# Performance work log

Hardware: AMD Instinct MI355X
Metric: run time of the kernel (lower is better)

Reference implementation:

```python
import jax, jax.numpy as jnp
import numpy as np

B, N, MAX_DEG = 256, 512, 6
F_IN, H = 62, 128  # layers = [62, 128, 128]
NUM_DEG = MAX_DEG + 1  # degree buckets 0..6


def gather_neighbors(atoms, edges, maskvalue):
    # atoms [B,N,F], edges [B,N,D] with -1 padding -> [B,N,D,F]
    idx = jnp.maximum(edges, 0)
    neigh = jax.vmap(lambda a, e: a[e])(atoms, idx)
    return jnp.where(edges[..., None] < 0, jnp.asarray(maskvalue, atoms.dtype), neigh)


def nfp_conv(atoms, edges, W, b):
    # W [NUM_DEG, F_in, F_out], b [NUM_DEG, F_out]
    deg = jnp.sum(edges >= 0, axis=-1)  # [B,N]
    neigh = gather_neighbors(atoms, edges, 0.0)
    summed = neigh.sum(axis=2) + atoms  # include self, [B,N,F_in]
    out = jnp.zeros(summed.shape[:2] + (W.shape[-1],), summed.dtype)
    for d in range(NUM_DEG):  # small fixed set of degree buckets
        h = jax.nn.sigmoid(summed @ W[d] + b[d])
        out = out + h * (deg == d)[..., None].astype(h.dtype)
    return out


def graph_pool(atoms, edges):
    # max over self + neighbors
    neigh = gather_neighbors(atoms, edges, -jnp.inf)
    allf = jnp.concatenate([atoms[:, :, None, :], neigh], axis=2)  # [B,N,D+1,F]
    return allf.max(axis=2)


def setup_inputs() -> dict:
    key = jax.random.key(0)
    ka, ke, km, k0, k1, k2, k3 = jax.random.split(key, 7)
    a = jax.random.normal(ka, (B, N, F_IN), dtype=jnp.float32)
    e = jax.random.randint(ke, (B, N, MAX_DEG), 0, N, dtype=jnp.int32)
    # introduce -1 padding so atoms have varied degrees 0..6
    u = jax.random.uniform(km, (B, N, MAX_DEG))
    e = jnp.where(u < 0.6, e, -1).astype(jnp.int32)
    W0 = jax.random.normal(k0, (NUM_DEG, F_IN, H), dtype=jnp.float32) * 0.1
    b0 = jax.random.normal(k1, (NUM_DEG, H), dtype=jnp.float32) * 0.1
    W1 = jax.random.normal(k2, (NUM_DEG, H, H), dtype=jnp.float32) * 0.1
    b1 = jax.random.normal(k3, (NUM_DEG, H), dtype=jnp.float32) * 0.1
    return {"a": a, "e": e, "W0": W0, "b0": b0, "W1": W1, "b1": b1}


def reference(a, e, W0, b0, W1, b1):
    x = nfp_conv(a, e, W0, b0)
    x = graph_pool(x, e)
    x = nfp_conv(x, e, W1, b1)
    x = graph_pool(x, e)
    return x.sum(axis=1)  # SubgraphSum: [B, H]
```

## Files before the change

### kernel.cpp

```cpp
#include <hip/hip_runtime.h>
#include <math.h>

#define BB 256
#define NN 512
#define DD 6
#define F_IN 62
#define HH 128
#define ND 7
#define TOTAL (BB*NN)

typedef __bf16 bf16x8 __attribute__((ext_vector_type(8)));
typedef float f32x4 __attribute__((ext_vector_type(4)));

__device__ __forceinline__ unsigned short f2bf(float f) {
    unsigned u = __builtin_bit_cast(unsigned, f);
    u = (u + 0x7FFFu + ((u >> 16) & 1u)) >> 16;
    return (unsigned short)u;
}
__device__ __forceinline__ float lo2f(unsigned x) { return __builtin_bit_cast(float, x << 16); }
__device__ __forceinline__ float hi2f(unsigned x) { return __builtin_bit_cast(float, x & 0xFFFF0000u); }


__global__ void k_zero(unsigned int* ghist) {
    if (threadIdx.x < ND) ghist[threadIdx.x] = 0u;
}

__global__ __launch_bounds__(256) void k_hist(const int* __restrict__ e,
                                              int* __restrict__ deg,
                                              unsigned int* __restrict__ ghist) {
    __shared__ unsigned int lh[ND];
    int t = threadIdx.x;
    if (t < ND) lh[t] = 0u;
    __syncthreads();
    int u = blockIdx.x * 256 + t;
    int d = 0;
#pragma unroll
    for (int j = 0; j < DD; ++j) d += (e[u * DD + j] >= 0) ? 1 : 0;
    deg[u] = d;
    atomicAdd(&lh[d], 1u);
    __syncthreads();
    if (t < ND) atomicAdd(&ghist[t], lh[t]);
}

__global__ void k_scan(const unsigned int* __restrict__ ghist,
                       unsigned int* __restrict__ cursors) {
    unsigned int acc = 0;
    for (int d = 0; d < ND; ++d) { cursors[d] = acc; acc += ghist[d]; }
}

__global__ __launch_bounds__(256) void k_scatter(const int* __restrict__ deg,
                                                 int* __restrict__ order,
                                                 unsigned int* __restrict__ cursors) {
    __shared__ unsigned int lcnt[ND];
    __shared__ unsigned int lbase[ND];
    int t = threadIdx.x;
    if (t < ND) lcnt[t] = 0u;
    __syncthreads();
    int u = blockIdx.x * 256 + t;
    int d = deg[u];
    unsigned int r = atomicAdd(&lcnt[d], 1u);
    __syncthreads();
    if (t < ND) lbase[t] = atomicAdd(&cursors[t], lcnt[t]);
    __syncthreads();
    order[lbase[d] + r] = u;
}


__global__ __launch_bounds__(256) void k_prep_a(const float* __restrict__ a,
                                                unsigned short* __restrict__ Ap) {
    int u = blockIdx.x * 256 + threadIdx.x;
    int r = u >> 3;
    int c0 = (u & 7) * 8;
    unsigned short h[8];
#pragma unroll
    for (int i = 0; i < 8; ++i) {
        int c = c0 + i;
        h[i] = (c < F_IN) ? f2bf(a[(size_t)r * F_IN + c]) : (unsigned short)0;
    }
    uint4 p;
    p.x = (unsigned)h[0] | ((unsigned)h[1] << 16);
    p.y = (unsigned)h[2] | ((unsigned)h[3] << 16);
    p.z = (unsigned)h[4] | ((unsigned)h[5] << 16);
    p.w = (unsigned)h[6] | ((unsigned)h[7] << 16);
    *(uint4*)&Ap[(size_t)r * 64 + c0] = p;
}


__global__ void k_prep_wt(const float* __restrict__ W, unsigned short* __restrict__ WT,
                          int F, int K) {
    int n = blockIdx.x;
    int d = blockIdx.y;
    for (int k = threadIdx.x; k < K; k += 64) {
        float v = (k < F) ? W[((size_t)d * F + k) * HH + n] : 0.f;
        WT[((size_t)d * HH + n) * K + k] = f2bf(v);
    }
}


template<int KB>
__global__ __launch_bounds__(256, 3)
void k_conv_mfma(const unsigned short* __restrict__ Xp,
                 const int* __restrict__ e,
                 const unsigned short* __restrict__ WT,
                 const float* __restrict__ bias,
                 const int* __restrict__ order,
                 const int* __restrict__ deg,
                 unsigned short* __restrict__ Y) {
    constexpr int K = KB * 8;
    constexpr int LOGKB = (KB == 16) ? 4 : 3;
    __shared__ unsigned short sP[64 * 128];
    __shared__ int vT[64];
    __shared__ int degT[64];
    __shared__ int eT[64 * DD];

    const int t = threadIdx.x;
    const int l = t & 63;
    const int w = t >> 6;

    if (t < 64) {
        int v = order[blockIdx.x * 64 + t];
        vT[t] = v;
        degT[t] = deg[v];
    }
    __syncthreads();
    for (int i = t; i < 64 * DD; i += 256) eT[i] = e[vT[i / DD] * DD + (i % DD)];
    __syncthreads();

    for (int u = t; u < 64 * KB; u += 256) {
        const int kb = u & (KB - 1);
        const int n = u >> LOGKB;
        const int v = vT[n];
        const int nbase = v & ~(NN - 1);
        float s[8];
        {
            uint4 p = *(const uint4*)(Xp + (size_t)v * K + kb * 8);
            s[0] = lo2f(p.x); s[1] = hi2f(p.x); s[2] = lo2f(p.y); s[3] = hi2f(p.y);
            s[4] = lo2f(p.z); s[5] = hi2f(p.z); s[6] = lo2f(p.w); s[7] = hi2f(p.w);
        }
#pragma unroll
        for (int j = 0; j < DD; ++j) {
            int idx = eT[n * DD + j];
            if (idx >= 0) {
                uint4 p = *(const uint4*)(Xp + (size_t)(nbase + idx) * K + kb * 8);
                s[0] += lo2f(p.x); s[1] += hi2f(p.x); s[2] += lo2f(p.y); s[3] += hi2f(p.y);
                s[4] += lo2f(p.z); s[5] += hi2f(p.z); s[6] += lo2f(p.w); s[7] += hi2f(p.w);
            }
        }
        uint4 r;
        r.x = (unsigned)f2bf(s[0]) | ((unsigned)f2bf(s[1]) << 16);
        r.y = (unsigned)f2bf(s[2]) | ((unsigned)f2bf(s[3]) << 16);
        r.z = (unsigned)f2bf(s[4]) | ((unsigned)f2bf(s[5]) << 16);
        r.w = (unsigned)f2bf(s[6]) | ((unsigned)f2bf(s[7]) << 16);
        const int kbs = kb ^ (n & 7);
        *(uint4*)&sP[(n * KB + kbs) * 8] = r;
    }
    __syncthreads();

    const int dlo = degT[0];
    const int dhi = degT[63];
    const int lr = l & 15;
    const int lq = l >> 4;

    for (int d = dlo; d <= dhi; ++d) {
        bf16x8 bf[K / 32][2];
#pragma unroll
        for (int kk = 0; kk < K / 32; ++kk)
#pragma unroll
            for (int nb = 0; nb < 2; ++nb) {
                int ncol = w * 32 + nb * 16 + lr;
                int krow = kk * 32 + lq * 8;
                bf[kk][nb] = *(const bf16x8*)(WT + ((size_t)d * HH + ncol) * K + krow);
            }

        f32x4 acc[4][2];
#pragma unroll
        for (int mb = 0; mb < 4; ++mb)
#pragma unroll
            for (int nb = 0; nb < 2; ++nb) {
                f32x4 z = {0.f, 0.f, 0.f, 0.f};
                acc[mb][nb] = z;
            }

#pragma unroll
        for (int kk = 0; kk < K / 32; ++kk) {
#pragma unroll
            for (int mb = 0; mb < 4; ++mb) {
                int nrow = mb * 16 + lr;
                int kbp = kk * 4 + lq;
                int kbs = kbp ^ (nrow & 7);
                bf16x8 af = *(const bf16x8*)&sP[(nrow * KB + kbs) * 8];
                acc[mb][0] = __builtin_amdgcn_mfma_f32_16x16x32_bf16(af, bf[kk][0], acc[mb][0], 0, 0, 0);
                acc[mb][1] = __builtin_amdgcn_mfma_f32_16x16x32_bf16(af, bf[kk][1], acc[mb][1], 0, 0, 0);
            }
        }

        if (dlo == dhi) {
            __syncthreads();
#pragma unroll
            for (int mb = 0; mb < 4; ++mb)
#pragma unroll
                for (int nb = 0; nb < 2; ++nb) {
                    int col = w * 32 + nb * 16 + lr;
                    float bv = bias[d * HH + col];
#pragma unroll
                    for (int r = 0; r < 4; ++r) {
                        int n = mb * 16 + lq * 4 + r;
                        float z = 1.f / (1.f + __expf(-(acc[mb][nb][r] + bv)));
                        sP[n * HH + col] = f2bf(z);
                    }
                }
            __syncthreads();
            for (int u = t; u < 64 * HH / 8; u += 256) {
                int n = u >> 4;
                int c8 = (u & 15) * 8;
                uint4 p = *(const uint4*)&sP[n * HH + c8];
                *(uint4*)&Y[(size_t)vT[n] * HH + c8] = p;
            }
        } else {
#pragma unroll
            for (int mb = 0; mb < 4; ++mb)
#pragma unroll
                for (int nb = 0; nb < 2; ++nb) {
                    int col = w * 32 + nb * 16 + lr;
                    float bv = bias[d * HH + col];
#pragma unroll
                    for (int r = 0; r < 4; ++r) {
                        int n = mb * 16 + lq * 4 + r;
                        if (degT[n] == d) {
                            float z = 1.f / (1.f + __expf(-(acc[mb][nb][r] + bv)));
                            Y[(size_t)vT[n] * HH + col] = f2bf(z);
                        }
                    }
                }
        }
    }
}


__global__ __launch_bounds__(256) void k_pool_bf(const unsigned short* __restrict__ X,
                                                 const int* __restrict__ e,
                                                 unsigned short* __restrict__ P) {
    const int t = threadIdx.x;
    const int u = blockIdx.x * 16 + (t >> 4);
    const int c8 = (t & 15) * 8;
    const int nbase = u & ~(NN - 1);
    float m[8];
    {
        uint4 p = *(const uint4*)(X + (size_t)u * HH + c8);
        m[0] = lo2f(p.x); m[1] = hi2f(p.x); m[2] = lo2f(p.y); m[3] = hi2f(p.y);
        m[4] = lo2f(p.z); m[5] = hi2f(p.z); m[6] = lo2f(p.w); m[7] = hi2f(p.w);
    }
#pragma unroll
    for (int j = 0; j < DD; ++j) {
        int idx = e[u * DD + j];
        if (idx >= 0) {
            uint4 p = *(const uint4*)(X + (size_t)(nbase + idx) * HH + c8);
            m[0] = fmaxf(m[0], lo2f(p.x)); m[1] = fmaxf(m[1], hi2f(p.x));
            m[2] = fmaxf(m[2], lo2f(p.y)); m[3] = fmaxf(m[3], hi2f(p.y));
            m[4] = fmaxf(m[4], lo2f(p.z)); m[5] = fmaxf(m[5], hi2f(p.z));
            m[6] = fmaxf(m[6], lo2f(p.w)); m[7] = fmaxf(m[7], hi2f(p.w));
        }
    }
    uint4 r;
    r.x = (unsigned)f2bf(m[0]) | ((unsigned)f2bf(m[1]) << 16);
    r.y = (unsigned)f2bf(m[2]) | ((unsigned)f2bf(m[3]) << 16);
    r.z = (unsigned)f2bf(m[4]) | ((unsigned)f2bf(m[5]) << 16);
    r.w = (unsigned)f2bf(m[6]) | ((unsigned)f2bf(m[7]) << 16);
    *(uint4*)&P[(size_t)u * HH + c8] = r;
}


__global__ __launch_bounds__(256) void k_pool_sum_part(const unsigned short* __restrict__ X,
                                                       const int* __restrict__ e,
                                                       float* __restrict__ partial) {
    __shared__ float red[16][HH + 4];
    const int t = threadIdx.x;
    const int b = blockIdx.x >> 3;
    const int chunk = blockIdx.x & 7;
    const int slot = t >> 4;
    const int c8 = (t & 15) * 8;
    float acc[8];
#pragma unroll
    for (int i = 0; i < 8; ++i) acc[i] = 0.f;

    for (int n = chunk * 64 + slot; n < chunk * 64 + 64; n += 16) {
        int u = b * NN + n;
        float m[8];
        uint4 p = *(const uint4*)(X + (size_t)u * HH + c8);
        m[0] = lo2f(p.x); m[1] = hi2f(p.x); m[2] = lo2f(p.y); m[3] = hi2f(p.y);
        m[4] = lo2f(p.z); m[5] = hi2f(p.z); m[6] = lo2f(p.w); m[7] = hi2f(p.w);
#pragma unroll
        for (int j = 0; j < DD; ++j) {
            int idx = e[u * DD + j];
            if (idx >= 0) {
                uint4 q = *(const uint4*)(X + (size_t)(b * NN + idx) * HH + c8);
                m[0] = fmaxf(m[0], lo2f(q.x)); m[1] = fmaxf(m[1], hi2f(q.x));
                m[2] = fmaxf(m[2], lo2f(q.y)); m[3] = fmaxf(m[3], hi2f(q.y));
                m[4] = fmaxf(m[4], lo2f(q.z)); m[5] = fmaxf(m[5], hi2f(q.z));
                m[6] = fmaxf(m[6], lo2f(q.w)); m[7] = fmaxf(m[7], hi2f(q.w));
            }
        }
#pragma unroll
        for (int i = 0; i < 8; ++i) acc[i] += m[i];
    }
#pragma unroll
    for (int i = 0; i < 8; ++i) red[slot][c8 + i] = acc[i];
    __syncthreads();
    if (t < HH) {
        float s = 0.f;
#pragma unroll
        for (int k = 0; k < 16; ++k) s += red[k][t];
        partial[(size_t)blockIdx.x * HH + t] = s;
    }
}


__global__ __launch_bounds__(256) void k_sum_final(const float* __restrict__ partial,
                                                   float* __restrict__ out) {
    int g = blockIdx.x * 256 + threadIdx.x;
    int b = g >> 7;
    int c = g & 127;
    float s = 0.f;
#pragma unroll
    for (int k = 0; k < 8; ++k) s += partial[(size_t)(b * 8 + k) * HH + c];
    out[g] = s;
}


extern "C" void kernel_launch(void* const* d_in, const int* in_sizes, int n_in,
                              void* d_out, int out_size, void* d_ws, size_t ws_size,
                              hipStream_t stream) {
    const float* a  = (const float*)d_in[0];
    const int*   e  = (const int*)d_in[1];
    const float* W0 = (const float*)d_in[2];
    const float* b0 = (const float*)d_in[3];
    const float* W1 = (const float*)d_in[4];
    const float* b1 = (const float*)d_in[5];
    float* out = (float*)d_out;

    char* ws = (char*)d_ws;
    const size_t XB = (size_t)TOTAL * HH * 2;
    unsigned short* xbuf = (unsigned short*)ws;
    unsigned short* pbuf = (unsigned short*)(ws + XB);
    unsigned short* Ap   = (unsigned short*)(ws + 2 * XB);
    float* partial = (float*)Ap;
    unsigned short* WT0  = (unsigned short*)(ws + 2 * XB + (size_t)TOTAL * 64 * 2);
    unsigned short* WT1  = WT0 + (size_t)ND * HH * 64;
    char* ip = (char*)(WT1 + (size_t)ND * HH * 128);
    int* deg   = (int*)ip;
    int* order = (int*)(ip + (size_t)TOTAL * 4);
    unsigned int* ghist   = (unsigned int*)(ip + (size_t)TOTAL * 8);
    unsigned int* cursors = ghist + 8;

    hipLaunchKernelGGL(k_zero, dim3(1), dim3(64), 0, stream, ghist);
    hipLaunchKernelGGL(k_hist, dim3(TOTAL / 256), dim3(256), 0, stream, e, deg, ghist);
    hipLaunchKernelGGL(k_scan, dim3(1), dim3(1), 0, stream, ghist, cursors);
    hipLaunchKernelGGL(k_scatter, dim3(TOTAL / 256), dim3(256), 0, stream, deg, order, cursors);

    hipLaunchKernelGGL(k_prep_a, dim3(TOTAL * 8 / 256), dim3(256), 0, stream, a, Ap);
    hipLaunchKernelGGL(k_prep_wt, dim3(HH, ND), dim3(64), 0, stream, W0, WT0, F_IN, 64);
    hipLaunchKernelGGL(k_prep_wt, dim3(HH, ND), dim3(64), 0, stream, W1, WT1, HH, 128);

    hipLaunchKernelGGL((k_conv_mfma<8>),  dim3(TOTAL / 64), dim3(256), 0, stream,
                       Ap, e, WT0, b0, order, deg, xbuf);
    hipLaunchKernelGGL(k_pool_bf, dim3(TOTAL / 16), dim3(256), 0, stream, xbuf, e, pbuf);
    hipLaunchKernelGGL((k_conv_mfma<16>), dim3(TOTAL / 64), dim3(256), 0, stream,
                       pbuf, e, WT1, b1, order, deg, xbuf);
    hipLaunchKernelGGL(k_pool_sum_part, dim3(BB * 8), dim3(256), 0, stream, xbuf, e, partial);
    hipLaunchKernelGGL(k_sum_final, dim3(BB * HH / 256), dim3(256), 0, stream, partial, out);
}
```

Baseline: 170.5 us.

## Sort atoms by degree per batch and remap block IDs for XCD-local gathers

```diff
diff --git a/kernel.cpp b/kernel.cpp
--- a/kernel.cpp
+++ b/kernel.cpp
@@ -21,48 +21,28 @@
 __device__ __forceinline__ float hi2f(unsigned x) { return __builtin_bit_cast(float, x & 0xFFFF0000u); }
 
 
-__global__ void k_zero(unsigned int* ghist) {
-    if (threadIdx.x < ND) ghist[threadIdx.x] = 0u;
-}
-
-__global__ __launch_bounds__(256) void k_hist(const int* __restrict__ e,
-                                              int* __restrict__ deg,
-                                              unsigned int* __restrict__ ghist) {
+__global__ __launch_bounds__(512) void k_sort_batch(const int* __restrict__ e,
+                                                    int* __restrict__ deg,
+                                                    int* __restrict__ order) {
     __shared__ unsigned int lh[ND];
-    int t = threadIdx.x;
+    __shared__ unsigned int base[ND];
+    const int b = blockIdx.x;
+    const int t = threadIdx.x;
     if (t < ND) lh[t] = 0u;
     __syncthreads();
-    int u = blockIdx.x * 256 + t;
+    const int u = b * NN + t;
     int d = 0;
 #pragma unroll
     for (int j = 0; j < DD; ++j) d += (e[u * DD + j] >= 0) ? 1 : 0;
     deg[u] = d;
-    atomicAdd(&lh[d], 1u);
-    __syncthreads();
-    if (t < ND) atomicAdd(&ghist[t], lh[t]);
-}
-
-__global__ void k_scan(const unsigned int* __restrict__ ghist,
-                       unsigned int* __restrict__ cursors) {
-    unsigned int acc = 0;
-    for (int d = 0; d < ND; ++d) { cursors[d] = acc; acc += ghist[d]; }
-}
-
-__global__ __launch_bounds__(256) void k_scatter(const int* __restrict__ deg,
-                                                 int* __restrict__ order,
-                                                 unsigned int* __restrict__ cursors) {
-    __shared__ unsigned int lcnt[ND];
-    __shared__ unsigned int lbase[ND];
-    int t = threadIdx.x;
-    if (t < ND) lcnt[t] = 0u;
-    __syncthreads();
-    int u = blockIdx.x * 256 + t;
-    int d = deg[u];
-    unsigned int r = atomicAdd(&lcnt[d], 1u);
-    __syncthreads();
-    if (t < ND) lbase[t] = atomicAdd(&cursors[t], lcnt[t]);
-    __syncthreads();
-    order[lbase[d] + r] = u;
+    unsigned int r = atomicAdd(&lh[d], 1u);
+    __syncthreads();
+    if (t == 0) {
+        unsigned int acc = 0;
+        for (int k = 0; k < ND; ++k) { base[k] = acc; acc += lh[k]; }
+    }
+    __syncthreads();
+    order[b * NN + base[d] + r] = u;
 }
 
 
@@ -117,8 +97,15 @@
     const int l = t & 63;
     const int w = t >> 6;
 
+    const int bi = blockIdx.x;
+    const int x8 = bi & 7;
+    const int j = bi >> 3;
+    const int batch = x8 + 8 * (j >> 3);
+    const int tile = j & 7;
+    const int g0 = batch * NN + tile * 64;
+
     if (t < 64) {
-        int v = order[blockIdx.x * 64 + t];
+        int v = order[g0 + t];
         vT[t] = v;
         degT[t] = deg[v];
     }
@@ -138,8 +125,8 @@
             s[4] = lo2f(p.z); s[5] = hi2f(p.z); s[6] = lo2f(p.w); s[7] = hi2f(p.w);
         }
 #pragma unroll
-        for (int j = 0; j < DD; ++j) {
-            int idx = eT[n * DD + j];
+        for (int jj = 0; jj < DD; ++jj) {
+            int idx = eT[n * DD + jj];
             if (idx >= 0) {
                 uint4 p = *(const uint4*)(Xp + (size_t)(nbase + idx) * K + kb * 8);
                 s[0] += lo2f(p.x); s[1] += hi2f(p.x); s[2] += lo2f(p.y); s[3] += hi2f(p.y);
@@ -241,7 +228,12 @@
                                                  const int* __restrict__ e,
                                                  unsigned short* __restrict__ P) {
     const int t = threadIdx.x;
-    const int u = blockIdx.x * 16 + (t >> 4);
+    const int bi = blockIdx.x;
+    const int x8 = bi & 7;
+    const int j = bi >> 3;
+    const int batch = x8 + 8 * (j >> 5);
+    const int sub = j & 31;
+    const int u = batch * NN + sub * 16 + (t >> 4);
     const int c8 = (t & 15) * 8;
     const int nbase = u & ~(NN - 1);
     float m[8];
@@ -251,8 +243,8 @@
         m[4] = lo2f(p.z); m[5] = hi2f(p.z); m[6] = lo2f(p.w); m[7] = hi2f(p.w);
     }
 #pragma unroll
-    for (int j = 0; j < DD; ++j) {
-        int idx = e[u * DD + j];
+    for (int jj = 0; jj < DD; ++jj) {
+        int idx = e[u * DD + jj];
         if (idx >= 0) {
             uint4 p = *(const uint4*)(X + (size_t)(nbase + idx) * HH + c8);
             m[0] = fmaxf(m[0], lo2f(p.x)); m[1] = fmaxf(m[1], hi2f(p.x));
@@ -275,8 +267,11 @@
                                                        float* __restrict__ partial) {
     __shared__ float red[16][HH + 4];
     const int t = threadIdx.x;
-    const int b = blockIdx.x >> 3;
-    const int chunk = blockIdx.x & 7;
+    const int bi = blockIdx.x;
+    const int x8 = bi & 7;
+    const int j = bi >> 3;
+    const int b = x8 + 8 * (j >> 3);
+    const int chunk = j & 7;
     const int slot = t >> 4;
     const int c8 = (t & 15) * 8;
     float acc[8];
@@ -290,8 +285,8 @@
         m[0] = lo2f(p.x); m[1] = hi2f(p.x); m[2] = lo2f(p.y); m[3] = hi2f(p.y);
         m[4] = lo2f(p.z); m[5] = hi2f(p.z); m[6] = lo2f(p.w); m[7] = hi2f(p.w);
 #pragma unroll
-        for (int j = 0; j < DD; ++j) {
-            int idx = e[u * DD + j];
+        for (int jj = 0; jj < DD; ++jj) {
+            int idx = e[u * DD + jj];
             if (idx >= 0) {
                 uint4 q = *(const uint4*)(X + (size_t)(b * NN + idx) * HH + c8);
                 m[0] = fmaxf(m[0], lo2f(q.x)); m[1] = fmaxf(m[1], hi2f(q.x));
@@ -310,7 +305,7 @@
         float s = 0.f;
 #pragma unroll
         for (int k = 0; k < 16; ++k) s += red[k][t];
-        partial[(size_t)blockIdx.x * HH + t] = s;
+        partial[(size_t)(b * 8 + chunk) * HH + t] = s;
     }
 }
 
@@ -349,13 +344,8 @@
     char* ip = (char*)(WT1 + (size_t)ND * HH * 128);
     int* deg   = (int*)ip;
     int* order = (int*)(ip + (size_t)TOTAL * 4);
-    unsigned int* ghist   = (unsigned int*)(ip + (size_t)TOTAL * 8);
-    unsigned int* cursors = ghist + 8;
-
-    hipLaunchKernelGGL(k_zero, dim3(1), dim3(64), 0, stream, ghist);
-    hipLaunchKernelGGL(k_hist, dim3(TOTAL / 256), dim3(256), 0, stream, e, deg, ghist);
-    hipLaunchKernelGGL(k_scan, dim3(1), dim3(1), 0, stream, ghist, cursors);
-    hipLaunchKernelGGL(k_scatter, dim3(TOTAL / 256), dim3(256), 0, stream, deg, order, cursors);
+
+    hipLaunchKernelGGL(k_sort_batch, dim3(BB), dim3(NN), 0, stream, e, deg, order);
 
     hipLaunchKernelGGL(k_prep_a, dim3(TOTAL * 8 / 256), dim3(256), 0, stream, a, Ap);
     hipLaunchKernelGGL(k_prep_wt, dim3(HH, ND), dim3(64), 0, stream, W0, WT0, F_IN, 64);
```

Measured after the change: 163.4 us. -4.1%, faster.
